# Kernel optimization log

Measured on AMD Instinct MI355X. Metric: run time of the kernel, lower is better.

The kernel has to match this reference:

```python
import jax, jax.numpy as jnp
import numpy as np

A, Bc, C, D = 32, 16, 16, 16
K, PAD = 3, 1
KK = K * K
KKA = KK * A            # 288
KKA2 = KKA // 2 + 1     # 145
BSZ, H, W = 4, 14, 14


def unfold(x, k, pad):
    # torch F.unfold ordering: channel-major, kernel-minor -> matches patches
    p = jax.lax.conv_general_dilated_patches(
        x, (k, k), (1, 1), padding=((pad, pad), (pad, pad)),
        dimension_numbers=("NCHW", "OIHW", "NCHW"))
    b, ckk, h, w = p.shape
    return p.reshape(b, ckk, h * w)


def freq_filter(x, cw):
    # x: [bl, kkA, B, D]; shared complex filter over all B splits (Frequency)
    xf = jnp.fft.rfft(x.astype(jnp.float32), axis=1, norm='ortho')  # [bl,kkA2,B,D]
    wc = cw[..., 0] + 1j * cw[..., 1]                               # [kkA2, D]
    y = jnp.fft.irfft(xf * wc[None, :, None, :], n=x.shape[1], axis=1, norm='ortho')
    return y + x


def spatial_gate(logit, gamma, beta, w, bias):
    # logit: [bl, kkA, B]; shared Spatial module applied per B split (vectorized)
    bl, kka, nb = logit.shape
    g = logit.reshape(bl, KK, A, nb)
    mu = g.mean(axis=2, keepdims=True)
    var = g.var(axis=2, keepdims=True)
    g = (g - mu) / jnp.sqrt(var + 1e-5) * gamma[None, None, :, None] + beta[None, None, :, None]
    # conv1d with kernel size 1 == channel mixing over kk
    out = jnp.einsum('oi,biaj->boaj', w, g) + bias[None, :, None, None]
    out = jax.nn.gelu(out, approximate=False)
    return out.reshape(bl, kka, nb) + logit  # residual inside Spatial


def setup_inputs():
    key = jax.random.key(0)
    ks = jax.random.split(key, 8)
    return {
        "a": jax.random.uniform(ks[0], (BSZ, A, H, W), jnp.float32) + 0.1,
        "pose": jax.random.normal(ks[1], (BSZ, A * C, H, W), jnp.float32),
        "mpose_w": jax.random.normal(ks[2], (Bc * D, C), jnp.float32) * 0.05,
        "mpose_b": jnp.zeros((Bc * D,), jnp.float32),
        "cpose2_w": jax.random.normal(ks[3], (Bc, C), jnp.float32) * 0.05,
        "cpose2_b": jnp.zeros((Bc,), jnp.float32),
        "complex_weight": jax.random.normal(ks[4], (KKA2, C, 2), jnp.float32) * 0.02,
        "ln_gamma": jnp.ones((A,), jnp.float32),
        "ln_beta": jnp.zeros((A,), jnp.float32),
        "sp_w": jax.random.normal(ks[5], (KK, KK), jnp.float32) * 0.1,
        "sp_b": jnp.ones((KK,), jnp.float32),
    }


def reference(a, pose, mpose_w, mpose_b, cpose2_w, cpose2_b, complex_weight,
              ln_gamma, ln_beta, sp_w, sp_b):
    b, _, h, w = a.shape
    # ---- unfold pose: [b, A*C*kk, l] -> [b*l, kkA, C]
    pu = unfold(pose, K, PAD)
    l = pu.shape[-1]
    pu = pu.reshape(b, A, C, KK, l).transpose(0, 4, 3, 1, 2).reshape(b * l, KKA, C)
    # ---- pose transform + frequency filter
    p = jax.nn.gelu(pu @ mpose_w.T + mpose_b, approximate=False)
    p = freq_filter(p.reshape(b * l, KKA, Bc, D), complex_weight)
    pose_out = p.reshape(b, l, KKA, Bc, D)
    # ---- routing logits: linear + (spatial gate + residual) added to logit
    logit = pu @ cpose2_w.T + cpose2_b                      # [bl, kkA, B]
    logit = logit + spatial_gate(logit, ln_gamma, ln_beta, sp_w, sp_b)
    r = jax.nn.softmax(logit, axis=2).reshape(b, l, KKA, Bc)
    # ---- unfold activations: [b, l, kkA, 1]
    au = unfold(a, K, PAD).reshape(b, A, KK, l).transpose(0, 3, 2, 1).reshape(b, l, KKA, 1)
    ar = au * r                                             # [b,l,kkA,B]
    ar_sum = ar.sum(axis=2, keepdims=True)                  # [b,l,1,B]
    coeff = (ar / ar_sum)[..., None]                        # [b,l,kkA,B,1]
    a_out = (ar_sum / au.sum(axis=2, keepdims=True)).squeeze(2)  # [b,l,B]
    a_out = a_out.transpose(0, 2, 1).reshape(b, Bc, h, w)
    po = (coeff * pose_out).sum(axis=2).reshape(b, l, Bc * D)
    po = po.transpose(0, 2, 1).reshape(b, Bc * D, h, w)
    return a_out, po
```

## Files before the change

### kernel.cpp

```cpp
#include <hip/hip_runtime.h>
#include <math.h>


typedef __attribute__((ext_vector_type(8))) short bf16x8;
typedef __attribute__((ext_vector_type(4))) float f32x4;

__device__ inline float4 ld4(const float* p) { return *reinterpret_cast<const float4*>(p); }
__device__ inline void st4(float* p, float4 v) { *reinterpret_cast<float4*>(p) = v; }
__device__ inline unsigned short f2bf(float f) {
  union { float f; unsigned int i; } v; v.f = f;
  unsigned int r = v.i + 0x7FFFu + ((v.i >> 16) & 1u);
  return (unsigned short)(r >> 16);
}
__device__ inline float gelu_f(float v) {
  float u = v * 0.70710678118654752f;
  float au = fabsf(u);
  float t = __builtin_amdgcn_rcpf(fmaf(0.3275911f, au, 1.f));
  float poly = t * fmaf(t, fmaf(t, fmaf(t, fmaf(t, 1.061405429f, -1.453152027f),
                                        1.421413741f), -0.284496736f),
                        0.254829592f);
  float e = __expf(-u * u);
  float r = fmaf(-poly, e, 1.f);
  float erfv = copysignf(r, u);
  return 0.5f * v * (1.f + erfv);
}

__global__ __launch_bounds__(256) void k_prep(
    const float* __restrict__ cw, const float* __restrict__ pose,
    const float* __restrict__ a_img, unsigned short* __restrict__ ws_H,
    float* __restrict__ poseT, float* __restrict__ aT) {
  int bid = blockIdx.x, tid = threadIdx.x;
  if (bid < 96) {
    __shared__ float s_h2[576];
    __shared__ float s_cs[288], s_sn[288], s_wr[145], s_wi[145];
    int d = bid / 6, chunk = bid % 6;
    for (int m = tid; m < 288; m += 256) {
      float sn, cs;
      sincosf((float)m * (6.283185307179586f / 288.f), &sn, &cs);
      s_cs[m] = cs; s_sn[m] = sn;
    }
    for (int f = tid; f < 145; f += 256) {
      s_wr[f] = cw[(f * 16 + d) * 2 + 0];
      s_wi[f] = cw[(f * 16 + d) * 2 + 1];
    }
    __syncthreads();
    for (int t = tid; t < 288; t += 256) {
      float acc = s_wr[0] + ((t & 1) ? -s_wr[144] : s_wr[144]);
      for (int f = 1; f < 144; ++f) {
        int m = (f * t) % 288;
        acc = fmaf(2.f * s_wr[f], s_cs[m], acc);
        acc = fmaf(-2.f * s_wi[f], s_sn[m], acc);
      }
      float h = acc * (1.f / 288.f);
      s_h2[t] = h;
      s_h2[t + 288] = h;
    }
    __syncthreads();
    for (int e = tid; e < 13824; e += 256) {
      int j = e & 7, l = (e >> 3) & 63;
      int kk = (e >> 9) % 9, mtl = (e >> 9) / 9;
      int mt = chunk * 3 + mtl;
      int m = l & 15, g = l >> 4;
      int n = kk * 32 + g * 8 + j, t = mt * 16 + m;
      float v = s_h2[n - t + 288] + ((n == t) ? 1.f : 0.f);
      ws_H[d * 82944 + ((mt * 9 + kk) * 64 + l) * 8 + j] = f2bf(v);
    }
  } else {
    __shared__ float s[32 * 201];
    int tb = bid - 96;
    int b = tb / 17, ch = tb % 17;
    const float* src = (ch < 16) ? (pose + (b * 512 + ch * 32) * 196)
                                 : (a_img + b * 32 * 196);
    for (int e = tid; e < 6272; e += 256) {
      int c = e / 196, l = e - c * 196;
      s[c * 201 + l] = src[e];
    }
    __syncthreads();
    if (ch < 16) {
      float* dst = poseT + b * 196 * 512 + ch * 32;
      for (int e = tid; e < 6272; e += 256) {
        int l = e >> 5, c = e & 31;
        dst[l * 512 + c] = s[c * 201 + l];
      }
    } else {
      float* dst = aT + b * 196 * 32;
      for (int e = tid; e < 6272; e += 256) {
        int l = e >> 5, c = e & 31;
        dst[l * 32 + c] = s[c * 201 + l];
      }
    }
  }
}

__global__ __launch_bounds__(256) void k_rowprep(
    const float* __restrict__ poseT, const float* __restrict__ aT,
    const float* __restrict__ cpose2_w, const float* __restrict__ cpose2_b,
    const float* __restrict__ ln_g, const float* __restrict__ ln_b,
    const float* __restrict__ sp_w, const float* __restrict__ sp_b,
    float* __restrict__ out_a, unsigned short* __restrict__ ws_pu,
    unsigned short* __restrict__ ws_cb) {
  __shared__ __align__(16) float s_pu[288 * 20];
#define s_l2 s_pu
  __shared__ __align__(16) float s_lg[288 * 20];
  __shared__ float s_au[288];
  __shared__ float s_mu[144], s_rs[144];
  __shared__ float s_ga[32], s_be[32];
  __shared__ float s_part[256], s_pau[16];
  __shared__ float s_as[16];

  int bid = blockIdx.x;
  int x = bid & 7, j = bid >> 3;
  int o = x + 8 * (j % 13);
  if (o >= 98) return;
  int row = o * 8 + (j / 13);

  int tid = threadIdx.x;
  int b = row / 196, loc = row % 196, i0 = loc / 14, j0 = loc % 14;
  int b_ = tid & 15;

  if (tid < 32) { s_ga[tid] = ln_g[tid]; s_be[tid] = ln_b[tid]; }

  float wcol[16];
#pragma unroll
  for (int q = 0; q < 4; ++q) {
    float4 v = ld4(&cpose2_w[b_ * 16 + 4 * q]);
    wcol[4 * q] = v.x; wcol[4 * q + 1] = v.y;
    wcol[4 * q + 2] = v.z; wcol[4 * q + 3] = v.w;
  }
  float cbv = cpose2_b[b_];

  const float* pT = poseT + b * 196 * 512;
  for (int e = tid; e < 1152; e += 256) {
    int q = e & 3, n = e >> 2;
    int kk = n >> 5, a = n & 31;
    int ki = (kk * 11) >> 5, kj = kk - 3 * ki;
    int yy = i0 + ki - 1, xx = j0 + kj - 1;
    float4 v = make_float4(0.f, 0.f, 0.f, 0.f);
    if ((unsigned)yy < 14u && (unsigned)xx < 14u)
      v = ld4(&pT[(yy * 14 + xx) * 512 + a * 16 + q * 4]);
    st4(&s_pu[n * 20 + q * 4], v);
  }
  const float* aTb = aT + b * 196 * 32;
  for (int n = tid; n < 288; n += 256) {
    int kk = n >> 5, a = n & 31;
    int ki = (kk * 11) >> 5, kj = kk - 3 * ki;
    int yy = i0 + ki - 1, xx = j0 + kj - 1;
    float v = 0.f;
    if ((unsigned)yy < 14u && (unsigned)xx < 14u)
      v = aTb[(yy * 14 + xx) * 32 + a];
    s_au[n] = v;
  }
  __syncthreads();

  for (int e = tid; e < 4608; e += 256) {
    int jj = e & 7, l2 = (e >> 3) & 31, mt = e >> 8;
    int m = l2 & 15, c = (l2 >> 4) * 8 + jj;
    ws_pu[row * 4608 + e] = f2bf(s_pu[(mt * 16 + m) * 20 + c]);
  }

  {
    int n0 = tid >> 4;
#pragma unroll 3
    for (int k = 0; k < 18; ++k) {
      int n = n0 + 16 * k;
      const float* pr = &s_pu[n * 20];
      float acc = cbv;
#pragma unroll
      for (int q = 0; q < 4; ++q) {
        float4 p = ld4(pr + 4 * q);
        acc += p.x * wcol[4 * q] + p.y * wcol[4 * q + 1] +
               p.z * wcol[4 * q + 2] + p.w * wcol[4 * q + 3];
      }
      s_lg[n * 20 + b_] = acc;
    }
  }
  __syncthreads();

  if (tid < 144) {
    int kk = tid >> 4, B = tid & 15;
    float s = 0.f, s2 = 0.f;
    for (int a = 0; a < 32; ++a) {
      float v = s_lg[(kk * 32 + a) * 20 + B];
      s += v; s2 += v * v;
    }
    float mu = s * (1.f / 32.f);
    float var = s2 * (1.f / 32.f) - mu * mu;
    s_mu[tid] = mu;
    s_rs[tid] = rsqrtf(var + 1e-5f);
  } else if (tid < 160) {
    int t2 = tid - 144;
    float p = 0.f;
    for (int i = 0; i < 18; ++i) p += s_au[t2 * 18 + i];
    s_pau[t2] = p;
  }
  __syncthreads();

  {
    float mu9[9], rs9[9];
#pragma unroll
    for (int i2 = 0; i2 < 9; ++i2) {
      mu9[i2] = s_mu[i2 * 16 + b_];
      rs9[i2] = s_rs[i2 * 16 + b_];
    }
#pragma unroll
    for (int half = 0; half < 2; ++half) {
      int a = (tid >> 4) + 16 * half;
      float ga = s_ga[a], be = s_be[a];
      float gn[9], lg9[9];
#pragma unroll
      for (int i2 = 0; i2 < 9; ++i2) {
        float v = s_lg[(i2 * 32 + a) * 20 + b_];
        lg9[i2] = v;
        gn[i2] = (v - mu9[i2]) * rs9[i2] * ga + be;
      }
#pragma unroll
      for (int oo = 0; oo < 9; ++oo) {
        float acc = sp_b[oo];
#pragma unroll
        for (int i2 = 0; i2 < 9; ++i2) acc += sp_w[oo * 9 + i2] * gn[i2];
        s_l2[(oo * 32 + a) * 20 + b_] = 2.f * lg9[oo] + gelu_f(acc);
      }
    }
  }
  __syncthreads();

  for (int n = tid; n < 288; n += 256) {
    float v[16];
#pragma unroll
    for (int q = 0; q < 4; ++q) {
      float4 t = ld4(&s_l2[n * 20 + 4 * q]);
      v[4 * q] = t.x; v[4 * q + 1] = t.y; v[4 * q + 2] = t.z; v[4 * q + 3] = t.w;
    }
    float m = v[0];
#pragma unroll
    for (int e = 1; e < 16; ++e) m = fmaxf(m, v[e]);
    float s = 0.f;
#pragma unroll
    for (int e = 0; e < 16; ++e) { v[e] = __expf(v[e] - m); s += v[e]; }
    float inv = 1.f / s;
#pragma unroll
    for (int q = 0; q < 4; ++q)
      st4(&s_l2[n * 20 + 4 * q],
          make_float4(v[4 * q] * inv, v[4 * q + 1] * inv, v[4 * q + 2] * inv,
                      v[4 * q + 3] * inv));
  }
  __syncthreads();

  {
    int sl = tid >> 4;
    float part = 0.f;
#pragma unroll 3
    for (int i = 0; i < 18; ++i) {
      int n = sl * 18 + i;
      part += s_au[n] * s_l2[n * 20 + b_];
    }
    s_part[tid] = part;
  }
  __syncthreads();

  if (tid < 16) {
    float s = 0.f;
#pragma unroll
    for (int q = 0; q < 16; ++q) s += s_part[tid + 16 * q];
    s_as[tid] = s;
    float aus = 0.f;
#pragma unroll
    for (int q = 0; q < 16; ++q) aus += s_pau[q];
    out_a[(b * 16 + tid) * 196 + loc] = s / aus;
  }
  __syncthreads();

  {
    float inv_as = 1.f / s_as[(tid >> 3) & 15];
    for (int e = tid; e < 4608; e += 256) {
      int jj = e & 7, B = (e >> 3) & 15, g2 = (e >> 7) & 3, kk = e >> 9;
      int n = kk * 32 + g2 * 8 + jj;
      float v = s_au[n] * s_l2[n * 20 + B] * inv_as;
      ws_cb[row * 4608 + e] = f2bf(v);
    }
  }
#undef s_l2
}

__global__ __launch_bounds__(256, 3) void k_gterm(
    const unsigned short* __restrict__ ws_H,
    const unsigned short* __restrict__ ws_pu,
    const unsigned short* __restrict__ ws_cb,
    const float* __restrict__ mpose_w, const float* __restrict__ mpose_b,
    float* __restrict__ out_po) {
  int bid = blockIdx.x;
  int xcd = bid & 7, q = bid >> 3;
  int k13 = q % 13, d = q / 13;
  int ro = xcd + 8 * k13;
  if (ro >= 98) return;

  int tid = threadIdx.x;
  int w = tid >> 6, l = tid & 63;
  int row0 = ro * 8 + w * 2, row1 = row0 + 1;
  int b_ = l & 15, g = l >> 4;

  const bf16x8 z8 = {0, 0, 0, 0, 0, 0, 0, 0};
  const f32x4 zf = {0.f, 0.f, 0.f, 0.f};

  bf16x8 bmw = z8;
  if (g < 2) {
    const float* mp = mpose_w + (b_ * 16 + d) * 16 + g * 8;
#pragma unroll
    for (int jj = 0; jj < 8; ++jj) bmw[jj] = (short)f2bf(mp[jj]);
  }
  float mb = mpose_b[b_ * 16 + d];
  f32x4 mbv = {mb, mb, mb, mb};

  union CU { uint4 u; bf16x8 v; };
  CU c0[9], c1[9];
  {
    const uint4* gC0 = (const uint4*)ws_cb + row0 * 576;
    const uint4* gC1 = (const uint4*)ws_cb + row1 * 576;
#pragma unroll
    for (int kk = 0; kk < 9; ++kk) {
      c0[kk].u = gC0[kk * 64 + l];
      c1[kk].u = gC1[kk * 64 + l];
    }
#pragma unroll
    for (int kk = 0; kk < 9; ++kk) {
      asm volatile("" : "+v"(c0[kk].u.x), "+v"(c0[kk].u.y),
                        "+v"(c0[kk].u.z), "+v"(c0[kk].u.w));
      asm volatile("" : "+v"(c1[kk].u.x), "+v"(c1[kk].u.y),
                        "+v"(c1[kk].u.z), "+v"(c1[kk].u.w));
    }
  }
  const bf16x8* aP0 = (const bf16x8*)ws_pu + row0 * 576;
  const bf16x8* aP1 = (const bf16x8*)ws_pu + row1 * 576;
  const bf16x8* aH = (const bf16x8*)ws_H + d * 10368;

  bf16x8 an0 = z8, an1 = z8;
  if (g < 2) { an0 = aP0[l]; an1 = aP1[l]; }

  float po0 = 0.f, po1 = 0.f;
  for (int mt = 0; mt < 18; ++mt) {
    bf16x8 h[9];
#pragma unroll
    for (int kk = 0; kk < 9; ++kk) h[kk] = aH[(mt * 9 + kk) * 64 + l];
    bf16x8 a0 = an0, a1 = an1;
    if (mt < 17 && g < 2) {
      an0 = aP0[(mt + 1) * 32 + l];
      an1 = aP1[(mt + 1) * 32 + l];
    }
    f32x4 xp0 = __builtin_amdgcn_mfma_f32_16x16x32_bf16(a0, bmw, mbv, 0, 0, 0);
    f32x4 xp1 = __builtin_amdgcn_mfma_f32_16x16x32_bf16(a1, bmw, mbv, 0, 0, 0);
    f32x4 g0 = zf, g1 = zf;
#pragma unroll
    for (int kk = 0; kk < 9; ++kk) {
      g0 = __builtin_amdgcn_mfma_f32_16x16x32_bf16(h[kk], c0[kk].v, g0, 0, 0, 0);
      g1 = __builtin_amdgcn_mfma_f32_16x16x32_bf16(h[kk], c1[kk].v, g1, 0, 0, 0);
    }
#pragma unroll
    for (int r = 0; r < 4; ++r) {
      po0 += g0[r] * gelu_f(xp0[r]);
      po1 += g1[r] * gelu_f(xp1[r]);
    }
  }

  po0 += __shfl_xor(po0, 16);
  po0 += __shfl_xor(po0, 32);
  po1 += __shfl_xor(po1, 16);
  po1 += __shfl_xor(po1, 32);
  if (l < 16) {
    int bb = row0 / 196, lc0 = row0 % 196, lc1 = row1 % 196;
    out_po[((bb * 256) + l * 16 + d) * 196 + lc0] = po0;
    out_po[((bb * 256) + l * 16 + d) * 196 + lc1] = po1;
  }
}

extern "C" void kernel_launch(void* const* d_in, const int* in_sizes, int n_in,
                              void* d_out, int out_size, void* d_ws, size_t ws_size,
                              hipStream_t stream) {
  const float* a_img    = (const float*)d_in[0];
  const float* pose     = (const float*)d_in[1];
  const float* mpose_w  = (const float*)d_in[2];
  const float* mpose_b  = (const float*)d_in[3];
  const float* cpose2_w = (const float*)d_in[4];
  const float* cpose2_b = (const float*)d_in[5];
  const float* cw       = (const float*)d_in[6];
  const float* ln_g     = (const float*)d_in[7];
  const float* ln_b     = (const float*)d_in[8];
  const float* sp_w     = (const float*)d_in[9];
  const float* sp_b     = (const float*)d_in[10];

  float* out = (float*)d_out;
  float* poseT  = (float*)d_ws;
  float* aT     = poseT + 4 * 196 * 512;
  unsigned short* ws_H  = (unsigned short*)(aT + 4 * 196 * 32);
  unsigned short* ws_pu = ws_H + 16 * 82944;
  unsigned short* ws_cb = ws_pu + 784 * 4608;

  hipLaunchKernelGGL(k_prep, dim3(164), dim3(256), 0, stream,
                     cw, pose, a_img, ws_H, poseT, aT);
  hipLaunchKernelGGL(k_rowprep, dim3(832), dim3(256), 0, stream,
                     poseT, aT, cpose2_w, cpose2_b, ln_g, ln_b, sp_w, sp_b,
                     out, ws_pu, ws_cb);
  hipLaunchKernelGGL(k_gterm, dim3(1664), dim3(256), 0, stream,
                     ws_H, ws_pu, ws_cb, mpose_w, mpose_b, out + 12544);
}
```

Before: 109.5 us.

## Switch gterm matmuls to 32x32x16 MFMA with row-pair packed layouts

Reorganizes the H, pose and coefficient workspace layouts so the gterm kernel can use 32x32x16 bf16 MFMA. Two spatial rows are packed into the 32-wide output dimension, so one wave handles a pair with a single accumulator instead of two 16x16 chains. Occupancy hint is lowered to 2 to make room for the larger register footprint. The aim is fewer MFMA issues and fewer redundant H fragment loads, at the cost of more registers and a cross-lane reduction over 16 outputs per lane.

```diff
diff --git a/kernel.cpp b/kernel.cpp
--- a/kernel.cpp
+++ b/kernel.cpp
@@ -3,7 +3,7 @@
 
 
 typedef __attribute__((ext_vector_type(8))) short bf16x8;
-typedef __attribute__((ext_vector_type(4))) float f32x4;
+typedef __attribute__((ext_vector_type(16))) float f32x16;
 
 __device__ inline float4 ld4(const float* p) { return *reinterpret_cast<const float4*>(p); }
 __device__ inline void st4(float* p, float4 v) { *reinterpret_cast<float4*>(p) = v; }
@@ -58,12 +58,13 @@
     __syncthreads();
     for (int e = tid; e < 13824; e += 256) {
       int j = e & 7, l = (e >> 3) & 63;
-      int kk = (e >> 9) % 9, mtl = (e >> 9) / 9;
-      int mt = chunk * 3 + mtl;
-      int m = l & 15, g = l >> 4;
-      int n = kk * 32 + g * 8 + j, t = mt * 16 + m;
+      int idx = e >> 9;
+      int mtnc = chunk * 27 + idx;
+      int mt32 = mtnc / 18, nc = mtnc % 18;
+      int t = mt32 * 32 + (l & 31);
+      int n = nc * 16 + (l >> 5) * 8 + j;
       float v = s_h2[n - t + 288] + ((n == t) ? 1.f : 0.f);
-      ws_H[d * 82944 + ((mt * 9 + kk) * 64 + l) * 8 + j] = f2bf(v);
+      ws_H[d * 82944 + chunk * 13824 + e] = f2bf(v);
     }
   } else {
     __shared__ float s[32 * 201];
@@ -153,9 +154,9 @@
   __syncthreads();
 
   for (int e = tid; e < 4608; e += 256) {
-    int jj = e & 7, l2 = (e >> 3) & 31, mt = e >> 8;
-    int m = l2 & 15, c = (l2 >> 4) * 8 + jj;
-    ws_pu[row * 4608 + e] = f2bf(s_pu[(mt * 16 + m) * 20 + c]);
+    int jj = e & 7, l = (e >> 3) & 63, mt32 = e >> 9;
+    int t = mt32 * 32 + (l & 31), c = (l >> 5) * 8 + jj;
+    ws_pu[row * 4608 + e] = f2bf(s_pu[t * 20 + c]);
   }
 
   {
@@ -272,17 +273,21 @@
 
   {
     float inv_as = 1.f / s_as[(tid >> 3) & 15];
+    unsigned short* dst = ws_cb + (row >> 1) * 9216;
+    int rbit = (row & 1) << 4;
     for (int e = tid; e < 4608; e += 256) {
-      int jj = e & 7, B = (e >> 3) & 15, g2 = (e >> 7) & 3, kk = e >> 9;
-      int n = kk * 32 + g2 * 8 + jj;
+      int jj = e & 7, li = (e >> 3) & 31, nc = e >> 8;
+      int l = (li & 15) | rbit | ((li >> 4) << 5);
+      int n = nc * 16 + (li >> 4) * 8 + jj;
+      int B = li & 15;
       float v = s_au[n] * s_l2[n * 20 + B] * inv_as;
-      ws_cb[row * 4608 + e] = f2bf(v);
+      dst[nc * 512 + l * 8 + jj] = f2bf(v);
     }
   }
 #undef s_l2
 }
 
-__global__ __launch_bounds__(256, 3) void k_gterm(
+__global__ __launch_bounds__(256, 2) void k_gterm(
     const unsigned short* __restrict__ ws_H,
     const unsigned short* __restrict__ ws_pu,
     const unsigned short* __restrict__ ws_cb,
@@ -296,79 +301,90 @@
 
   int tid = threadIdx.x;
   int w = tid >> 6, l = tid & 63;
-  int row0 = ro * 8 + w * 2, row1 = row0 + 1;
-  int b_ = l & 15, g = l >> 4;
+  int pair = ro * 4 + w;
+  int row0 = pair * 2, row1 = row0 + 1;
+  int hi = l >> 5, l31 = l & 31;
 
   const bf16x8 z8 = {0, 0, 0, 0, 0, 0, 0, 0};
-  const f32x4 zf = {0.f, 0.f, 0.f, 0.f};
-
-  bf16x8 bmw = z8;
-  if (g < 2) {
-    const float* mp = mpose_w + (b_ * 16 + d) * 16 + g * 8;
-#pragma unroll
-    for (int jj = 0; jj < 8; ++jj) bmw[jj] = (short)f2bf(mp[jj]);
-  }
-  float mb = mpose_b[b_ * 16 + d];
-  f32x4 mbv = {mb, mb, mb, mb};
+  const f32x16 zf16 = {0.f, 0.f, 0.f, 0.f, 0.f, 0.f, 0.f, 0.f,
+                       0.f, 0.f, 0.f, 0.f, 0.f, 0.f, 0.f, 0.f};
+
+  bf16x8 mwA = z8;
+  if (l31 < 16) {
+    const float* mp = mpose_w + (l31 * 16 + d) * 16 + hi * 8;
+#pragma unroll
+    for (int jj = 0; jj < 8; ++jj) mwA[jj] = (short)f2bf(mp[jj]);
+  }
+  float mb8[8];
+#pragma unroll
+  for (int r = 0; r < 8; ++r)
+    mb8[r] = mpose_b[((r & 3) + 8 * (r >> 2) + 4 * hi) * 16 + d];
 
   union CU { uint4 u; bf16x8 v; };
-  CU c0[9], c1[9];
+  CU cA[18];
   {
-    const uint4* gC0 = (const uint4*)ws_cb + row0 * 576;
-    const uint4* gC1 = (const uint4*)ws_cb + row1 * 576;
-#pragma unroll
-    for (int kk = 0; kk < 9; ++kk) {
-      c0[kk].u = gC0[kk * 64 + l];
-      c1[kk].u = gC1[kk * 64 + l];
-    }
-#pragma unroll
-    for (int kk = 0; kk < 9; ++kk) {
-      asm volatile("" : "+v"(c0[kk].u.x), "+v"(c0[kk].u.y),
-                        "+v"(c0[kk].u.z), "+v"(c0[kk].u.w));
-      asm volatile("" : "+v"(c1[kk].u.x), "+v"(c1[kk].u.y),
-                        "+v"(c1[kk].u.z), "+v"(c1[kk].u.w));
-    }
-  }
-  const bf16x8* aP0 = (const bf16x8*)ws_pu + row0 * 576;
-  const bf16x8* aP1 = (const bf16x8*)ws_pu + row1 * 576;
-  const bf16x8* aH = (const bf16x8*)ws_H + d * 10368;
-
-  bf16x8 an0 = z8, an1 = z8;
-  if (g < 2) { an0 = aP0[l]; an1 = aP1[l]; }
-
-  float po0 = 0.f, po1 = 0.f;
-  for (int mt = 0; mt < 18; ++mt) {
-    bf16x8 h[9];
-#pragma unroll
-    for (int kk = 0; kk < 9; ++kk) h[kk] = aH[(mt * 9 + kk) * 64 + l];
-    bf16x8 a0 = an0, a1 = an1;
-    if (mt < 17 && g < 2) {
-      an0 = aP0[(mt + 1) * 32 + l];
-      an1 = aP1[(mt + 1) * 32 + l];
-    }
-    f32x4 xp0 = __builtin_amdgcn_mfma_f32_16x16x32_bf16(a0, bmw, mbv, 0, 0, 0);
-    f32x4 xp1 = __builtin_amdgcn_mfma_f32_16x16x32_bf16(a1, bmw, mbv, 0, 0, 0);
-    f32x4 g0 = zf, g1 = zf;
-#pragma unroll
-    for (int kk = 0; kk < 9; ++kk) {
-      g0 = __builtin_amdgcn_mfma_f32_16x16x32_bf16(h[kk], c0[kk].v, g0, 0, 0, 0);
-      g1 = __builtin_amdgcn_mfma_f32_16x16x32_bf16(h[kk], c1[kk].v, g1, 0, 0, 0);
-    }
-#pragma unroll
-    for (int r = 0; r < 4; ++r) {
-      po0 += g0[r] * gelu_f(xp0[r]);
-      po1 += g1[r] * gelu_f(xp1[r]);
-    }
-  }
-
-  po0 += __shfl_xor(po0, 16);
-  po0 += __shfl_xor(po0, 32);
-  po1 += __shfl_xor(po1, 16);
-  po1 += __shfl_xor(po1, 32);
-  if (l < 16) {
+    const uint4* gC = (const uint4*)ws_cb + pair * 1152;
+#pragma unroll
+    for (int nc = 0; nc < 18; ++nc) cA[nc].u = gC[nc * 64 + l];
+#pragma unroll
+    for (int nc = 0; nc < 18; ++nc)
+      asm volatile("" : "+v"(cA[nc].u.x), "+v"(cA[nc].u.y),
+                        "+v"(cA[nc].u.z), "+v"(cA[nc].u.w));
+  }
+  const bf16x8* gH = (const bf16x8*)(ws_H + d * 82944);
+  const bf16x8* gP0 = (const bf16x8*)(ws_pu + row0 * 4608);
+  const bf16x8* gP1 = (const bf16x8*)(ws_pu + row1 * 4608);
+
+  float poA[16];
+#pragma unroll
+  for (int r = 0; r < 16; ++r) poA[r] = 0.f;
+
+  for (int mt = 0; mt < 9; ++mt) {
+    bf16x8 p0 = gP0[mt * 64 + l];
+    bf16x8 p1 = gP1[mt * 64 + l];
+    bf16x8 hA_[9];
+#pragma unroll
+    for (int nc = 0; nc < 9; ++nc) hA_[nc] = gH[(mt * 18 + nc) * 64 + l];
+    f32x16 xp0 = __builtin_amdgcn_mfma_f32_32x32x16_bf16(mwA, p0, zf16, 0, 0, 0);
+    f32x16 xp1 = __builtin_amdgcn_mfma_f32_32x32x16_bf16(mwA, p1, zf16, 0, 0, 0);
+    f32x16 gg = zf16;
+#pragma unroll
+    for (int nc = 0; nc < 9; ++nc)
+      gg = __builtin_amdgcn_mfma_f32_32x32x16_bf16(cA[nc].v, hA_[nc], gg, 0, 0, 0);
+    bf16x8 hB_[9];
+#pragma unroll
+    for (int nc = 0; nc < 9; ++nc) hB_[nc] = gH[(mt * 18 + 9 + nc) * 64 + l];
+    float xu[16];
+#pragma unroll
+    for (int r = 0; r < 8; ++r) {
+      xu[r] = gelu_f(xp0[r] + mb8[r]);
+      xu[r + 8] = gelu_f(xp1[r] + mb8[r]);
+    }
+#pragma unroll
+    for (int nc = 0; nc < 9; ++nc)
+      gg = __builtin_amdgcn_mfma_f32_32x32x16_bf16(cA[9 + nc].v, hB_[nc], gg, 0, 0, 0);
+#pragma unroll
+    for (int r = 0; r < 16; ++r) poA[r] = fmaf(gg[r], xu[r], poA[r]);
+  }
+
+#pragma unroll
+  for (int r = 0; r < 16; ++r) {
+    float v = poA[r];
+    v += __shfl_xor(v, 1);
+    v += __shfl_xor(v, 2);
+    v += __shfl_xor(v, 4);
+    v += __shfl_xor(v, 8);
+    v += __shfl_xor(v, 16);
+    poA[r] = v;
+  }
+  if (l31 == 0) {
     int bb = row0 / 196, lc0 = row0 % 196, lc1 = row1 % 196;
-    out_po[((bb * 256) + l * 16 + d) * 196 + lc0] = po0;
-    out_po[((bb * 256) + l * 16 + d) * 196 + lc1] = po1;
+#pragma unroll
+    for (int r = 0; r < 16; ++r) {
+      int rb = (r & 3) + 8 * (r >> 2) + 4 * hi;
+      int B = rb & 15, rw = rb >> 4;
+      out_po[((bb * 256) + B * 16 + d) * 196 + (rw ? lc1 : lc0)] = poA[r];
+    }
   }
 }
 
```

Result: slower. 184.7 us (+68.7%).
